# Optimization experiments

Hardware: AMD Instinct MI355X
Metric: run time of the kernel (lower is better)

## Reference

```python
import jax, jax.numpy as jnp
import numpy as np

N = 50000          # nodes
E = 800000         # edges (before self loops)
D = 128            # features (in = out)
H = 2              # heads
L = 2              # layers
NEG_SLOPE = 0.2    # GATConv leaky_relu slope


def setup_inputs() -> dict:
    key = jax.random.key(0)
    k = jax.random.split(key, 7)
    x = jax.random.normal(k[0], (N, D), dtype=jnp.float32)
    edge_index = jax.random.randint(k[1], (2, E), 0, N, dtype=jnp.int64)
    # Per-layer GATConv params (lin shared for src/dst as in PyG single-input mode)
    s = 1.0 / np.sqrt(D)
    W = jax.random.uniform(k[2], (L, D, H * D), dtype=jnp.float32, minval=-s, maxval=s)
    att_src = jax.random.uniform(k[3], (L, H, D), dtype=jnp.float32, minval=-s, maxval=s)
    att_dst = jax.random.uniform(k[4], (L, H, D), dtype=jnp.float32, minval=-s, maxval=s)
    bias = jnp.zeros((L, D), dtype=jnp.float32)
    return {"x": x, "edge_index": edge_index, "W": W,
            "att_src": att_src, "att_dst": att_dst, "bias": bias}


def _gat_layer(x, src, dst, W, a_src, a_dst, b):
    n = x.shape[0]
    h = (x @ W).reshape(n, H, D)                    # [N,H,C]
    alpha_s = jnp.sum(h * a_src[None], axis=-1)     # [N,H]
    alpha_d = jnp.sum(h * a_dst[None], axis=-1)     # [N,H]
    e = jax.nn.leaky_relu(alpha_s[src] + alpha_d[dst], NEG_SLOPE)  # [E',H]
    # segment softmax over incoming edges of each dst node
    m = jax.ops.segment_max(e, dst, num_segments=n)
    e = jnp.exp(e - m[dst])
    z = jax.ops.segment_sum(e, dst, num_segments=n)
    alpha = e / (z[dst] + 1e-16)                    # [E',H]
    msg = h[src] * alpha[:, :, None]                # [E',H,C]
    out = jax.ops.segment_sum(msg, dst, num_segments=n)  # [N,H,C]
    return out.mean(axis=1) + b                     # concat=False -> head mean


def _l2_normalize(x, eps=1e-12):
    nrm = jnp.sqrt(jnp.sum(x * x, axis=1, keepdims=True))
    return x / jnp.maximum(nrm, eps)


def reference(x, edge_index, W, att_src, att_dst, bias):
    n = x.shape[0]
    loop = jnp.arange(n, dtype=edge_index.dtype)
    src = jnp.concatenate([edge_index[0], loop])    # add self loops
    dst = jnp.concatenate([edge_index[1], loop])
    h = x
    for l in range(L):
        h = _gat_layer(h, src, dst, W[l], att_src[l], att_dst[l], bias[l])
        h = _l2_normalize(h)
    return h
```

## Files before the change

kernel.cpp:

```cpp
#include <hip/hip_runtime.h>


using short8  = __attribute__((ext_vector_type(8))) short;
using float4v = __attribute__((ext_vector_type(4))) float;

static __device__ __forceinline__ float bf2f(unsigned int u16) {
    union { unsigned int i; float f; } v; v.i = u16 << 16; return v.f;
}
static __device__ __forceinline__ float bflo(unsigned int p){
    union { unsigned int i; float f; } v; v.i = p << 16; return v.f;
}
static __device__ __forceinline__ float bfhi(unsigned int p){
    union { unsigned int i; float f; } v; v.i = p & 0xffff0000u; return v.f;
}
static __device__ __forceinline__ unsigned short f2bf(float f) {
    union { float f; unsigned int i; } v; v.f = f;
    unsigned int x = v.i;
    x += 0x7fffu + ((x >> 16) & 1u);
    return (unsigned short)(x >> 16);
}
static __device__ __forceinline__ float leaky(float x){ return x > 0.f ? x : 0.2f * x; }

__global__ __launch_bounds__(256) void k_probe_zero(const unsigned int* __restrict__ xw,
                                                    const int* __restrict__ ei,
                                                    int* __restrict__ flags,
                                                    int* __restrict__ cursor, int N) {
    int i = blockIdx.x * 256 + threadIdx.x;
    if (i < N) cursor[i] = 0;
    if (blockIdx.x == 0) {
        __shared__ int insane, oddnz;
        int t = threadIdx.x;
        if (t == 0) { insane = 0; oddnz = 0; }
        __syncthreads();
        unsigned int w = xw[t];
        if (((w >> 7) & 0xFFu) >= 154u) atomicOr(&insane, 1);
        if (ei[2 * t + 1] != 0) atomicOr(&oddnz, 1);
        __syncthreads();
        if (t == 0) { flags[0] = insane ? 1 : 0; flags[1] = oddnz ? 0 : 1; }
    }
}

__global__ __launch_bounds__(256) void k_transpose(const void* __restrict__ W,
                                                   unsigned short* __restrict__ WT,
                                                   const int* __restrict__ flags) {
    int fx = flags[0];
    int idx = blockIdx.x * 256 + threadIdx.x;
    int layer = idx >> 15;
    int rem = idx & 32767;
    int k = rem >> 8, n = rem & 255;
    int srci = layer * 32768 + k * 256 + n;
    unsigned short v;
    if (fx) v = f2bf(((const float*)W)[srci]);
    else    v = ((const unsigned short*)W)[srci];
    WT[layer * 32768 + n * 128 + k] = v;
}

__global__ __launch_bounds__(256) void k_gemm_alpha(const void* __restrict__ X,
                                                    const unsigned short* __restrict__ WT,
                                                    const void* __restrict__ atts,
                                                    const void* __restrict__ attd,
                                                    int layer,
                                                    unsigned short* __restrict__ Hb,
                                                    float* __restrict__ as_, float* __restrict__ ad_,
                                                    int N, const int* __restrict__ flags) {
    __shared__ float lds_s[4][16], lds_d[4][16];
    int fx = flags[0];
    int mt = blockIdx.x;
    int wave = threadIdx.x >> 6;
    int lane = threadIdx.x & 63;
    int r16 = lane & 15, quad = lane >> 4;
    int m0 = mt << 4;
    int arow = m0 + r16; if (arow >= N) arow = N - 1;
    short8 a[4];
    if (fx) {
        const float* Xf = (const float*)X;
#pragma unroll
        for (int kk = 0; kk < 4; kk++) {
            const float4v* pv = (const float4v*)(Xf + (size_t)arow * 128 + kk * 32 + quad * 8);
            float4v lo = pv[0], hi = pv[1];
            short8 t;
            t[0] = (short)f2bf(lo[0]); t[1] = (short)f2bf(lo[1]);
            t[2] = (short)f2bf(lo[2]); t[3] = (short)f2bf(lo[3]);
            t[4] = (short)f2bf(hi[0]); t[5] = (short)f2bf(hi[1]);
            t[6] = (short)f2bf(hi[2]); t[7] = (short)f2bf(hi[3]);
            a[kk] = t;
        }
    } else {
        const unsigned short* Xh = (const unsigned short*)X;
#pragma unroll
        for (int kk = 0; kk < 4; kk++)
            a[kk] = *(const short8*)(Xh + (size_t)arow * 128 + kk * 32 + quad * 8);
    }
    int head = wave >> 1;
    float ps[4] = {0.f, 0.f, 0.f, 0.f}, pd[4] = {0.f, 0.f, 0.f, 0.f};
#pragma unroll
    for (int nn = 0; nn < 4; nn++) {
        int nt = wave * 4 + nn;
        float4v acc = {0.f, 0.f, 0.f, 0.f};
#pragma unroll
        for (int kk = 0; kk < 4; kk++) {
            short8 b = *(const short8*)(WT + (nt * 16 + r16) * 128 + kk * 32 + quad * 8);
            acc = __builtin_amdgcn_mfma_f32_16x16x32_bf16(a[kk], b, acc, 0, 0, 0);
        }
        int col = nt * 16 + r16;
        int c = col & 127;
        float sa, da;
        if (fx) {
            sa = ((const float*)atts)[layer * 256 + head * 128 + c];
            da = ((const float*)attd)[layer * 256 + head * 128 + c];
        } else {
            sa = bf2f(((const unsigned short*)atts)[layer * 256 + head * 128 + c]);
            da = bf2f(((const unsigned short*)attd)[layer * 256 + head * 128 + c]);
        }
#pragma unroll
        for (int r = 0; r < 4; r++) {
            int row = m0 + quad * 4 + r;
            if (row < N) Hb[(size_t)row * 256 + col] = f2bf(acc[r]);
            ps[r] += acc[r] * sa;
            pd[r] += acc[r] * da;
        }
    }
#pragma unroll
    for (int m = 1; m < 16; m <<= 1) {
#pragma unroll
        for (int r = 0; r < 4; r++) {
            ps[r] += __shfl_xor(ps[r], m);
            pd[r] += __shfl_xor(pd[r], m);
        }
    }
    if (r16 == 0) {
#pragma unroll
        for (int r = 0; r < 4; r++) {
            lds_s[wave][quad * 4 + r] = ps[r];
            lds_d[wave][quad * 4 + r] = pd[r];
        }
    }
    __syncthreads();
    if (threadIdx.x < 16) {
        int row = m0 + threadIdx.x;
        if (row < N) {
            float2 sv = { lds_s[0][threadIdx.x] + lds_s[1][threadIdx.x],
                          lds_s[2][threadIdx.x] + lds_s[3][threadIdx.x] };
            float2 dv = { lds_d[0][threadIdx.x] + lds_d[1][threadIdx.x],
                          lds_d[2][threadIdx.x] + lds_d[3][threadIdx.x] };
            *(float2*)(as_ + 2 * row) = sv;
            *(float2*)(ad_ + 2 * row) = dv;
        }
    }
}

static __device__ __forceinline__ int edge_dst(const int* ei, int E, int i, int is64) {
    return is64 ? ei[2 * E + 2 * i] : ei[E + i];
}
static __device__ __forceinline__ int edge_src(const int* ei, int E, int i, int is64) {
    return is64 ? ei[2 * i] : ei[i];
}

__global__ __launch_bounds__(256) void k_count(const int* __restrict__ ei, int E, int N,
                                               const int* __restrict__ flags, int* deg) {
    int i = blockIdx.x * 256 + threadIdx.x;
    if (i >= E + N) return;
    int dst;
    if (i < E) { dst = edge_dst(ei, E, i, flags[1]); if ((unsigned)dst >= (unsigned)N) dst = 0; }
    else dst = i - E;
    atomicAdd(&deg[dst], 1);
}

__global__ __launch_bounds__(1024) void k_scan1(const int* __restrict__ deg, int* __restrict__ excl,
                                                int* __restrict__ bsum, int n) {
    __shared__ int buf[1024];
    int t = threadIdx.x;
    int i = blockIdx.x * 1024 + t;
    int v = (i < n) ? deg[i] : 0;
    int x = v; buf[t] = v; __syncthreads();
    for (int off = 1; off < 1024; off <<= 1) {
        int add = (t >= off) ? buf[t - off] : 0;
        __syncthreads();
        x += add; buf[t] = x;
        __syncthreads();
    }
    if (i < n) excl[i] = x - v;
    if (t == 1023) bsum[blockIdx.x] = x;
}

__global__ __launch_bounds__(256) void k_scan2(int* bsum, int nb) {
    __shared__ int buf[256];
    int t = threadIdx.x;
    int v = (t < nb) ? bsum[t] : 0;
    int x = v; buf[t] = v; __syncthreads();
    for (int off = 1; off < 256; off <<= 1) {
        int add = (t >= off) ? buf[t - off] : 0;
        __syncthreads();
        x += add; buf[t] = x;
        __syncthreads();
    }
    if (t < nb) bsum[t] = x - v;
    if (t == nb - 1) bsum[nb] = x;
}

__global__ __launch_bounds__(256) void k_scan3(int* __restrict__ rowptr, const int* __restrict__ bsum,
                                               int* __restrict__ cursor, int N) {
    int i = blockIdx.x * 256 + threadIdx.x;
    if (i < N) {
        int r = rowptr[i] + bsum[i >> 10];
        rowptr[i] = r;
        cursor[i] = r;
    } else if (i == N) {
        rowptr[N] = bsum[(N + 1023) >> 10];
    }
}

__global__ __launch_bounds__(256) void k_scatter(const int* __restrict__ ei, int E, int N,
                                                 const int* __restrict__ flags,
                                                 int* __restrict__ cursor, int* __restrict__ csr) {
    int i = blockIdx.x * 256 + threadIdx.x;
    if (i >= E + N) return;
    int src, dst;
    if (i < E) {
        int is64 = flags[1];
        src = edge_src(ei, E, i, is64);
        dst = edge_dst(ei, E, i, is64);
        if ((unsigned)src >= (unsigned)N) src = 0;
        if ((unsigned)dst >= (unsigned)N) dst = 0;
    } else src = dst = i - E;
    int pos = atomicAdd(&cursor[dst], 1);
    csr[pos] = src;
}

static __device__ __forceinline__ void acc8(float* A, float w, uint4 q) {
    A[0] += w * bflo(q.x); A[1] += w * bfhi(q.x);
    A[2] += w * bflo(q.y); A[3] += w * bfhi(q.y);
    A[4] += w * bflo(q.z); A[5] += w * bfhi(q.z);
    A[6] += w * bflo(q.w); A[7] += w * bfhi(q.w);
}

__global__ __launch_bounds__(256) void k_aggregate(const unsigned short* __restrict__ Hb,
                                                   const float* __restrict__ as_, const float* __restrict__ ad_,
                                                   const int* __restrict__ rowptr, const int* __restrict__ csr,
                                                   const void* __restrict__ bias, int layer,
                                                   const int* __restrict__ flags,
                                                   void* __restrict__ outp, int N, int EL) {
    int fx = flags[0];
    int n = blockIdx.x * 4 + (threadIdx.x >> 6);
    if (n >= N) return;
    int lane = threadIdx.x & 63;
    int g = lane >> 4;
    int gl = lane & 15;
    int start = rowptr[n], end = rowptr[n + 1];
    if (start < 0) start = 0;
    if (end > EL) end = EL;
    if (end < start) end = start;
    float2 adv = *(const float2*)(ad_ + 2 * n);
    float ad0 = adv.x, ad1 = adv.y;

    float acc0[8] = {0,0,0,0,0,0,0,0}, acc1[8] = {0,0,0,0,0,0,0,0};
    float z0, z1;
    int deg = end - start;

    if (deg <= 64) {
        int i = start + lane;
        bool act = i < end;
        int s = 0; float l0 = -1e30f, l1 = -1e30f;
        if (act) {
            s = csr[i]; if ((unsigned)s >= (unsigned)N) s = 0;
            float2 av = *(const float2*)(as_ + 2 * s);
            l0 = leaky(av.x + ad0); l1 = leaky(av.y + ad1);
        }
        float m0 = l0, m1 = l1;
#pragma unroll
        for (int m = 1; m < 64; m <<= 1) { m0 = fmaxf(m0, __shfl_xor(m0, m)); m1 = fmaxf(m1, __shfl_xor(m1, m)); }
        float w0 = act ? __expf(l0 - m0) : 0.f;
        float w1 = act ? __expf(l1 - m1) : 0.f;
        z0 = w0; z1 = w1;
#pragma unroll
        for (int m = 1; m < 64; m <<= 1) { z0 += __shfl_xor(z0, m); z1 += __shfl_xor(z1, m); }
#pragma unroll 2
        for (int j = 0; 4 * j < deg; j++) {
            int e = 4 * j + g;
            int sq    = __shfl(s, e);
            float wq0 = __shfl(w0, e);
            float wq1 = __shfl(w1, e);
            if (e < deg) {
                const unsigned short* row = Hb + ((size_t)sq << 8);
                uint4 q0 = *(const uint4*)(row + gl * 8);
                uint4 q1 = *(const uint4*)(row + 128 + gl * 8);
                acc8(acc0, wq0, q0);
                acc8(acc1, wq1, q1);
            }
        }
    } else {
        float m0 = -1e30f, m1 = -1e30f;
        for (int i = start + lane; i < end; i += 64) {
            int s = csr[i]; if ((unsigned)s >= (unsigned)N) s = 0;
            float2 av = *(const float2*)(as_ + 2 * s);
            m0 = fmaxf(m0, leaky(av.x + ad0));
            m1 = fmaxf(m1, leaky(av.y + ad1));
        }
#pragma unroll
        for (int m = 1; m < 64; m <<= 1) { m0 = fmaxf(m0, __shfl_xor(m0, m)); m1 = fmaxf(m1, __shfl_xor(m1, m)); }
        z0 = 0.f; z1 = 0.f;
        for (int t = start; t < end; t += 64) {
            int i = t + lane;
            int s = 0; float w0 = 0.f, w1 = 0.f;
            if (i < end) {
                s = csr[i]; if ((unsigned)s >= (unsigned)N) s = 0;
                float2 av = *(const float2*)(as_ + 2 * s);
                w0 = __expf(leaky(av.x + ad0) - m0);
                w1 = __expf(leaky(av.y + ad1) - m1);
                z0 += w0; z1 += w1;
            }
            int cnt = end - t; if (cnt > 64) cnt = 64;
            for (int j = 0; 4 * j < cnt; j++) {
                int e = 4 * j + g;
                int sq    = __shfl(s, e);
                float wq0 = __shfl(w0, e);
                float wq1 = __shfl(w1, e);
                if (e < cnt) {
                    const unsigned short* row = Hb + ((size_t)sq << 8);
                    uint4 q0 = *(const uint4*)(row + gl * 8);
                    uint4 q1 = *(const uint4*)(row + 128 + gl * 8);
                    acc8(acc0, wq0, q0);
                    acc8(acc1, wq1, q1);
                }
            }
        }
#pragma unroll
        for (int m = 1; m < 64; m <<= 1) { z0 += __shfl_xor(z0, m); z1 += __shfl_xor(z1, m); }
    }

    float inv0 = 1.f / (z0 + 1e-16f), inv1 = 1.f / (z1 + 1e-16f);
#pragma unroll
    for (int k = 0; k < 8; k++) {
        acc0[k] += __shfl_xor(acc0[k], 16); acc0[k] += __shfl_xor(acc0[k], 32);
        acc1[k] += __shfl_xor(acc1[k], 16); acc1[k] += __shfl_xor(acc1[k], 32);
    }

    float v[8];
    if (fx) {
        const float* bf = (const float*)bias + layer * 128 + gl * 8;
#pragma unroll
        for (int k = 0; k < 8; k++) v[k] = 0.5f * (acc0[k] * inv0 + acc1[k] * inv1) + bf[k];
    } else {
        const unsigned short* bh = (const unsigned short*)bias + layer * 128 + gl * 8;
        uint4 bv = *(const uint4*)bh;
        float bfv[8] = { bflo(bv.x), bfhi(bv.x), bflo(bv.y), bfhi(bv.y),
                         bflo(bv.z), bfhi(bv.z), bflo(bv.w), bfhi(bv.w) };
#pragma unroll
        for (int k = 0; k < 8; k++) v[k] = 0.5f * (acc0[k] * inv0 + acc1[k] * inv1) + bfv[k];
    }

    float ss = 0.f;
#pragma unroll
    for (int k = 0; k < 8; k++) ss += v[k] * v[k];
#pragma unroll
    for (int m = 1; m < 16; m <<= 1) ss += __shfl_xor(ss, m);
    float inv = 1.f / fmaxf(sqrtf(ss), 1e-12f);

    if (lane < 16) {
        if (fx) {
            float* op = (float*)outp + (size_t)n * 128 + gl * 8;
            float4 o0 = { v[0] * inv, v[1] * inv, v[2] * inv, v[3] * inv };
            float4 o1 = { v[4] * inv, v[5] * inv, v[6] * inv, v[7] * inv };
            *(float4*)op = o0;
            *(float4*)(op + 4) = o1;
        } else {
            unsigned short* op = (unsigned short*)outp + (size_t)n * 128 + gl * 8;
            uint4 pk;
            pk.x = (unsigned int)f2bf(v[0] * inv) | ((unsigned int)f2bf(v[1] * inv) << 16);
            pk.y = (unsigned int)f2bf(v[2] * inv) | ((unsigned int)f2bf(v[3] * inv) << 16);
            pk.z = (unsigned int)f2bf(v[4] * inv) | ((unsigned int)f2bf(v[5] * inv) << 16);
            pk.w = (unsigned int)f2bf(v[6] * inv) | ((unsigned int)f2bf(v[7] * inv) << 16);
            *(uint4*)op = pk;
        }
    }
}

extern "C" void kernel_launch(void* const* d_in, const int* in_sizes, int n_in,
                              void* d_out, int out_size, void* d_ws, size_t ws_size,
                              hipStream_t stream) {
    const void* x    = d_in[0];
    const int*  ei   = (const int*)d_in[1];
    const void* W    = d_in[2];
    const void* atts = d_in[3];
    const void* attd = d_in[4];
    const void* bias = d_in[5];

    int N = in_sizes[0] / 128;
    int E = in_sizes[1] / 2;
    int EL = E + N;

    char* p = (char*)d_ws;
    auto alloc = [&](size_t bytes) -> char* {
        char* q = p; p += (bytes + 255) & ~(size_t)255; return q;
    };
    int* flags   = (int*)alloc(256);
    int* bsum    = (int*)alloc(2048 * 4);
    int* rowptr  = (int*)alloc((size_t)(N + 1) * 4);
    int* cursor  = (int*)alloc((size_t)N * 4);
    float* as_   = (float*)alloc((size_t)N * 2 * 4);
    float* ad_   = (float*)alloc((size_t)N * 2 * 4);
    unsigned short* wt = (unsigned short*)alloc(2 * 256 * 128 * 2);
    int* csr     = (int*)alloc((size_t)EL * 4);
    unsigned short* hbuf = (unsigned short*)alloc((size_t)N * 256 * 2);

    k_probe_zero<<<(N + 255) / 256, 256, 0, stream>>>((const unsigned int*)x, ei, flags, cursor, N);
    k_count<<<(EL + 255) / 256, 256, 0, stream>>>(ei, E, N, flags, cursor);
    int nb = (N + 1023) / 1024;
    k_scan1<<<nb, 1024, 0, stream>>>(cursor, rowptr, bsum, N);
    k_scan2<<<1, 256, 0, stream>>>(bsum, nb);
    k_scan3<<<(N + 256) / 256, 256, 0, stream>>>(rowptr, bsum, cursor, N);
    k_scatter<<<(EL + 255) / 256, 256, 0, stream>>>(ei, E, N, flags, cursor, csr);
    k_transpose<<<256, 256, 0, stream>>>(W, wt, flags);

    int mtiles = (N + 15) / 16;
    for (int l = 0; l < 2; l++) {
        const void* xin = (l == 0) ? x : (const void*)d_out;
        k_gemm_alpha<<<mtiles, 256, 0, stream>>>(xin, wt + l * 32768, atts, attd, l,
                                                 hbuf, as_, ad_, N, flags);
        k_aggregate<<<(N + 3) / 4, 256, 0, stream>>>(hbuf, as_, ad_, rowptr, csr, bias, l, flags,
                                                     d_out, N, EL);
    }
}
```

Before: 388.8 us.

## Split aggregation into weight, sliced gather, and normalize kernels with sliced H layout

The GEMM now writes H in a column-sliced layout: eight slices of 32 bf16 values (16 channels × 2 heads) per node. The fused aggregate kernel is split into three kernels. k_weights computes normalized softmax weights per edge, k_gather launches 8 blocks per node group so each gathers one 64-byte slice, and k_norm does the L2 normalization afterwards. The intent is to shrink the gather working set per block so it stays in L2/cache, at the cost of extra launches, re-reading csr and weights eight times, and writing and rereading the output.

```diff
diff --git a/kernel.cpp b/kernel.cpp
--- a/kernel.cpp
+++ b/kernel.cpp
@@ -112,10 +112,11 @@
             sa = bf2f(((const unsigned short*)atts)[layer * 256 + head * 128 + c]);
             da = bf2f(((const unsigned short*)attd)[layer * 256 + head * 128 + c]);
         }
+        size_t sbase = (size_t)(nt & 7) * N * 32 + (nt >> 3) * 16 + r16;
 #pragma unroll
         for (int r = 0; r < 4; r++) {
             int row = m0 + quad * 4 + r;
-            if (row < N) Hb[(size_t)row * 256 + col] = f2bf(acc[r]);
+            if (row < N) Hb[sbase + (size_t)row * 32] = f2bf(acc[r]);
             ps[r] += acc[r] * sa;
             pd[r] += acc[r] * da;
         }
@@ -227,42 +228,26 @@
     csr[pos] = src;
 }
 
-static __device__ __forceinline__ void acc8(float* A, float w, uint4 q) {
-    A[0] += w * bflo(q.x); A[1] += w * bfhi(q.x);
-    A[2] += w * bflo(q.y); A[3] += w * bfhi(q.y);
-    A[4] += w * bflo(q.z); A[5] += w * bfhi(q.z);
-    A[6] += w * bflo(q.w); A[7] += w * bfhi(q.w);
-}
-
-__global__ __launch_bounds__(256) void k_aggregate(const unsigned short* __restrict__ Hb,
-                                                   const float* __restrict__ as_, const float* __restrict__ ad_,
-                                                   const int* __restrict__ rowptr, const int* __restrict__ csr,
-                                                   const void* __restrict__ bias, int layer,
-                                                   const int* __restrict__ flags,
-                                                   void* __restrict__ outp, int N, int EL) {
-    int fx = flags[0];
+__global__ __launch_bounds__(256) void k_weights(const float* __restrict__ as_, const float* __restrict__ ad_,
+                                                 const int* __restrict__ rowptr, const int* __restrict__ csr,
+                                                 float* __restrict__ wbuf, int N, int EL) {
     int n = blockIdx.x * 4 + (threadIdx.x >> 6);
     if (n >= N) return;
     int lane = threadIdx.x & 63;
-    int g = lane >> 4;
-    int gl = lane & 15;
     int start = rowptr[n], end = rowptr[n + 1];
     if (start < 0) start = 0;
     if (end > EL) end = EL;
     if (end < start) end = start;
     float2 adv = *(const float2*)(ad_ + 2 * n);
     float ad0 = adv.x, ad1 = adv.y;
-
-    float acc0[8] = {0,0,0,0,0,0,0,0}, acc1[8] = {0,0,0,0,0,0,0,0};
-    float z0, z1;
     int deg = end - start;
 
     if (deg <= 64) {
-        int i = start + lane;
-        bool act = i < end;
+        int e = start + lane;
+        bool act = e < end;
         int s = 0; float l0 = -1e30f, l1 = -1e30f;
         if (act) {
-            s = csr[i]; if ((unsigned)s >= (unsigned)N) s = 0;
+            s = csr[e]; if ((unsigned)s >= (unsigned)N) s = 0;
             float2 av = *(const float2*)(as_ + 2 * s);
             l0 = leaky(av.x + ad0); l1 = leaky(av.y + ad1);
         }
@@ -271,23 +256,11 @@
         for (int m = 1; m < 64; m <<= 1) { m0 = fmaxf(m0, __shfl_xor(m0, m)); m1 = fmaxf(m1, __shfl_xor(m1, m)); }
         float w0 = act ? __expf(l0 - m0) : 0.f;
         float w1 = act ? __expf(l1 - m1) : 0.f;
-        z0 = w0; z1 = w1;
+        float z0 = w0, z1 = w1;
 #pragma unroll
         for (int m = 1; m < 64; m <<= 1) { z0 += __shfl_xor(z0, m); z1 += __shfl_xor(z1, m); }
-#pragma unroll 2
-        for (int j = 0; 4 * j < deg; j++) {
-            int e = 4 * j + g;
-            int sq    = __shfl(s, e);
-            float wq0 = __shfl(w0, e);
-            float wq1 = __shfl(w1, e);
-            if (e < deg) {
-                const unsigned short* row = Hb + ((size_t)sq << 8);
-                uint4 q0 = *(const uint4*)(row + gl * 8);
-                uint4 q1 = *(const uint4*)(row + 128 + gl * 8);
-                acc8(acc0, wq0, q0);
-                acc8(acc1, wq1, q1);
-            }
-        }
+        float inv0 = 1.f / (z0 + 1e-16f), inv1 = 1.f / (z1 + 1e-16f);
+        if (act) { float2 o = { w0 * inv0, w1 * inv1 }; *(float2*)(wbuf + 2 * e) = o; }
     } else {
         float m0 = -1e30f, m1 = -1e30f;
         for (int i = start + lane; i < end; i += 64) {
@@ -298,80 +271,114 @@
         }
 #pragma unroll
         for (int m = 1; m < 64; m <<= 1) { m0 = fmaxf(m0, __shfl_xor(m0, m)); m1 = fmaxf(m1, __shfl_xor(m1, m)); }
-        z0 = 0.f; z1 = 0.f;
-        for (int t = start; t < end; t += 64) {
-            int i = t + lane;
-            int s = 0; float w0 = 0.f, w1 = 0.f;
-            if (i < end) {
-                s = csr[i]; if ((unsigned)s >= (unsigned)N) s = 0;
-                float2 av = *(const float2*)(as_ + 2 * s);
-                w0 = __expf(leaky(av.x + ad0) - m0);
-                w1 = __expf(leaky(av.y + ad1) - m1);
-                z0 += w0; z1 += w1;
-            }
-            int cnt = end - t; if (cnt > 64) cnt = 64;
-            for (int j = 0; 4 * j < cnt; j++) {
-                int e = 4 * j + g;
-                int sq    = __shfl(s, e);
-                float wq0 = __shfl(w0, e);
-                float wq1 = __shfl(w1, e);
-                if (e < cnt) {
-                    const unsigned short* row = Hb + ((size_t)sq << 8);
-                    uint4 q0 = *(const uint4*)(row + gl * 8);
-                    uint4 q1 = *(const uint4*)(row + 128 + gl * 8);
-                    acc8(acc0, wq0, q0);
-                    acc8(acc1, wq1, q1);
-                }
-            }
+        float z0 = 0.f, z1 = 0.f;
+        for (int i = start + lane; i < end; i += 64) {
+            int s = csr[i]; if ((unsigned)s >= (unsigned)N) s = 0;
+            float2 av = *(const float2*)(as_ + 2 * s);
+            z0 += __expf(leaky(av.x + ad0) - m0);
+            z1 += __expf(leaky(av.y + ad1) - m1);
         }
 #pragma unroll
         for (int m = 1; m < 64; m <<= 1) { z0 += __shfl_xor(z0, m); z1 += __shfl_xor(z1, m); }
-    }
-
-    float inv0 = 1.f / (z0 + 1e-16f), inv1 = 1.f / (z1 + 1e-16f);
-#pragma unroll
-    for (int k = 0; k < 8; k++) {
-        acc0[k] += __shfl_xor(acc0[k], 16); acc0[k] += __shfl_xor(acc0[k], 32);
-        acc1[k] += __shfl_xor(acc1[k], 16); acc1[k] += __shfl_xor(acc1[k], 32);
-    }
-
-    float v[8];
+        float inv0 = 1.f / (z0 + 1e-16f), inv1 = 1.f / (z1 + 1e-16f);
+        for (int i = start + lane; i < end; i += 64) {
+            int s = csr[i]; if ((unsigned)s >= (unsigned)N) s = 0;
+            float2 av = *(const float2*)(as_ + 2 * s);
+            float2 o = { __expf(leaky(av.x + ad0) - m0) * inv0,
+                         __expf(leaky(av.y + ad1) - m1) * inv1 };
+            *(float2*)(wbuf + 2 * i) = o;
+        }
+    }
+}
+
+__global__ __launch_bounds__(256) void k_gather(const unsigned short* __restrict__ Hb,
+                                                const float* __restrict__ wbuf,
+                                                const int* __restrict__ rowptr, const int* __restrict__ csr,
+                                                const void* __restrict__ bias, int layer,
+                                                const int* __restrict__ flags,
+                                                void* __restrict__ outp, int N, int EL) {
+    int fx = flags[0];
+    int slice = blockIdx.x & 7;
+    int n = (blockIdx.x >> 3) * 4 + (threadIdx.x >> 6);
+    if (n >= N) return;
+    int lane = threadIdx.x & 63;
+    int g = lane >> 3;
+    int sub = lane & 7;
+    int hsel = (lane >> 2) & 1;
+    int start = rowptr[n], end = rowptr[n + 1];
+    if (start < 0) start = 0;
+    if (end > EL) end = EL;
+    if (end < start) end = start;
+
+    const unsigned short* base = Hb + (size_t)slice * N * 32 + sub * 4;
+    float a0 = 0.f, a1 = 0.f, a2 = 0.f, a3 = 0.f;
+    for (int t = start; t < end; t += 8) {
+        int e = t + g;
+        if (e < end) {
+            int s = csr[e]; if ((unsigned)s >= (unsigned)N) s = 0;
+            float w = wbuf[2 * e + hsel];
+            uint2 q = *(const uint2*)(base + (size_t)s * 32);
+            a0 += w * bflo(q.x); a1 += w * bfhi(q.x);
+            a2 += w * bflo(q.y); a3 += w * bfhi(q.y);
+        }
+    }
+#pragma unroll
+    for (int m = 8; m < 64; m <<= 1) {
+        a0 += __shfl_xor(a0, m); a1 += __shfl_xor(a1, m);
+        a2 += __shfl_xor(a2, m); a3 += __shfl_xor(a3, m);
+    }
+    float v0 = 0.5f * (a0 + __shfl_xor(a0, 4));
+    float v1 = 0.5f * (a1 + __shfl_xor(a1, 4));
+    float v2 = 0.5f * (a2 + __shfl_xor(a2, 4));
+    float v3 = 0.5f * (a3 + __shfl_xor(a3, 4));
+
+    if (lane < 4) {
+        int c = slice * 16 + lane * 4;
+        float b0, b1, b2, b3;
+        if (fx) {
+            const float* bf = (const float*)bias + layer * 128 + c;
+            b0 = bf[0]; b1 = bf[1]; b2 = bf[2]; b3 = bf[3];
+        } else {
+            uint2 bv = *(const uint2*)((const unsigned short*)bias + layer * 128 + c);
+            b0 = bflo(bv.x); b1 = bfhi(bv.x); b2 = bflo(bv.y); b3 = bfhi(bv.y);
+        }
+        v0 += b0; v1 += b1; v2 += b2; v3 += b3;
+        if (fx) {
+            float4 o = { v0, v1, v2, v3 };
+            *(float4*)((float*)outp + (size_t)n * 128 + c) = o;
+        } else {
+            uint2 pk;
+            pk.x = (unsigned int)f2bf(v0) | ((unsigned int)f2bf(v1) << 16);
+            pk.y = (unsigned int)f2bf(v2) | ((unsigned int)f2bf(v3) << 16);
+            *(uint2*)((unsigned short*)outp + (size_t)n * 128 + c) = pk;
+        }
+    }
+}
+
+__global__ __launch_bounds__(256) void k_norm(void* __restrict__ outp,
+                                              const int* __restrict__ flags, int N) {
+    int fx = flags[0];
+    int n = blockIdx.x * 4 + (threadIdx.x >> 6);
+    if (n >= N) return;
+    int lane = threadIdx.x & 63;
+    float a, b;
     if (fx) {
-        const float* bf = (const float*)bias + layer * 128 + gl * 8;
-#pragma unroll
-        for (int k = 0; k < 8; k++) v[k] = 0.5f * (acc0[k] * inv0 + acc1[k] * inv1) + bf[k];
+        float2 v = *(float2*)((float*)outp + (size_t)n * 128 + lane * 2);
+        a = v.x; b = v.y;
     } else {
-        const unsigned short* bh = (const unsigned short*)bias + layer * 128 + gl * 8;
-        uint4 bv = *(const uint4*)bh;
-        float bfv[8] = { bflo(bv.x), bfhi(bv.x), bflo(bv.y), bfhi(bv.y),
-                         bflo(bv.z), bfhi(bv.z), bflo(bv.w), bfhi(bv.w) };
-#pragma unroll
-        for (int k = 0; k < 8; k++) v[k] = 0.5f * (acc0[k] * inv0 + acc1[k] * inv1) + bfv[k];
-    }
-
-    float ss = 0.f;
-#pragma unroll
-    for (int k = 0; k < 8; k++) ss += v[k] * v[k];
-#pragma unroll
-    for (int m = 1; m < 16; m <<= 1) ss += __shfl_xor(ss, m);
+        unsigned int p = *(unsigned int*)((unsigned short*)outp + (size_t)n * 128 + lane * 2);
+        a = bflo(p); b = bfhi(p);
+    }
+    float ss = a * a + b * b;
+#pragma unroll
+    for (int m = 1; m < 64; m <<= 1) ss += __shfl_xor(ss, m);
     float inv = 1.f / fmaxf(sqrtf(ss), 1e-12f);
-
-    if (lane < 16) {
-        if (fx) {
-            float* op = (float*)outp + (size_t)n * 128 + gl * 8;
-            float4 o0 = { v[0] * inv, v[1] * inv, v[2] * inv, v[3] * inv };
-            float4 o1 = { v[4] * inv, v[5] * inv, v[6] * inv, v[7] * inv };
-            *(float4*)op = o0;
-            *(float4*)(op + 4) = o1;
-        } else {
-            unsigned short* op = (unsigned short*)outp + (size_t)n * 128 + gl * 8;
-            uint4 pk;
-            pk.x = (unsigned int)f2bf(v[0] * inv) | ((unsigned int)f2bf(v[1] * inv) << 16);
-            pk.y = (unsigned int)f2bf(v[2] * inv) | ((unsigned int)f2bf(v[3] * inv) << 16);
-            pk.z = (unsigned int)f2bf(v[4] * inv) | ((unsigned int)f2bf(v[5] * inv) << 16);
-            pk.w = (unsigned int)f2bf(v[6] * inv) | ((unsigned int)f2bf(v[7] * inv) << 16);
-            *(uint4*)op = pk;
-        }
+    if (fx) {
+        float2 o = { a * inv, b * inv };
+        *(float2*)((float*)outp + (size_t)n * 128 + lane * 2) = o;
+    } else {
+        unsigned int pk = (unsigned int)f2bf(a * inv) | ((unsigned int)f2bf(b * inv) << 16);
+        *(unsigned int*)((unsigned short*)outp + (size_t)n * 128 + lane * 2) = pk;
     }
 }
 
@@ -401,6 +408,7 @@
     float* ad_   = (float*)alloc((size_t)N * 2 * 4);
     unsigned short* wt = (unsigned short*)alloc(2 * 256 * 128 * 2);
     int* csr     = (int*)alloc((size_t)EL * 4);
+    float* wbuf  = (float*)alloc((size_t)EL * 2 * 4);
     unsigned short* hbuf = (unsigned short*)alloc((size_t)N * 256 * 2);
 
     k_probe_zero<<<(N + 255) / 256, 256, 0, stream>>>((const unsigned int*)x, ei, flags, cursor, N);
@@ -413,11 +421,14 @@
     k_transpose<<<256, 256, 0, stream>>>(W, wt, flags);
 
     int mtiles = (N + 15) / 16;
+    int ngrp = (N + 3) / 4;
     for (int l = 0; l < 2; l++) {
         const void* xin = (l == 0) ? x : (const void*)d_out;
         k_gemm_alpha<<<mtiles, 256, 0, stream>>>(xin, wt + l * 32768, atts, attd, l,
                                                  hbuf, as_, ad_, N, flags);
-        k_aggregate<<<(N + 3) / 4, 256, 0, stream>>>(hbuf, as_, ad_, rowptr, csr, bias, l, flags,
-                                                     d_out, N, EL);
-    }
-}
+        k_weights<<<ngrp, 256, 0, stream>>>(as_, ad_, rowptr, csr, wbuf, N, EL);
+        k_gather<<<ngrp * 8, 256, 0, stream>>>(hbuf, wbuf, rowptr, csr, bias, l, flags,
+                                               d_out, N, EL);
+        k_norm<<<ngrp, 256, 0, stream>>>(d_out, flags, N);
+    }
+}
```

New measurement: 624.1 us. 60.5% more time.
